# Kernel tuning notes

Measured on AMD Instinct MI355X. Metric: run time of the kernel, lower is better.

## Reference

```python
import jax, jax.numpy as jnp
import numpy as np

B, C_IN, C_OUT = 4, 8, 8
P_IN, P_OUT = 16384, 4096
N_EVAL = 1_000_000
SPATIAL = 2
HID = 64
DECAY = (P_IN / 16) ** 2  # 1048576.0; bump support: ||z||^4 <= 1/DECAY -> ||z|| <= 1/32


def setup_inputs() -> dict:
    key = jax.random.key(0)
    ks = jax.random.split(key, 8)
    features = jax.random.normal(ks[0], (B, C_IN, P_IN), jnp.float32)
    # offsets inside the bump support (max ||z|| ~ 0.0283 < 0.03125 keeps 1 - DECAY*||z||^4 > 0)
    eval_locs = (jax.random.uniform(ks[1], (N_EVAL, SPATIAL), jnp.float32) * 2.0 - 1.0) * 0.02
    quad_weights = jax.random.uniform(ks[2], (P_IN,), jnp.float32, 0.5, 1.5) / P_IN
    # filter MLP: spatial_dim -> 64 -> 64 -> C_IN*C_OUT, Sin activations, no bias
    W0 = jax.random.normal(ks[3], (SPATIAL, HID), jnp.float32) / np.float32(np.sqrt(SPATIAL))
    W1 = jax.random.normal(ks[4], (HID, HID), jnp.float32) / np.float32(np.sqrt(HID))
    W2 = jax.random.normal(ks[5], (HID, C_IN * C_OUT), jnp.float32) / np.float32(np.sqrt(HID))
    eval_idx_out = jnp.sort(jax.random.randint(ks[6], (N_EVAL,), 0, P_OUT, jnp.int32))
    eval_idx_in = jax.random.randint(ks[7], (N_EVAL,), 0, P_IN, jnp.int32)
    return dict(features=features, eval_locs=eval_locs, quad_weights=quad_weights,
                W0=W0, W1=W1, W2=W2, eval_idx_out=eval_idx_out, eval_idx_in=eval_idx_in)


def reference(features, eval_locs, quad_weights, W0, W1, W2, eval_idx_out, eval_idx_in):
    # per-eval-point filter G(z): (N, C_in, C_out)
    h = jnp.sin(eval_locs @ W0)
    h = jnp.sin(h @ W1)
    filt = (h @ W2).reshape(-1, C_IN, C_OUT)
    # bump(z) = exp(1 - 1/(1 - decay*||z||^4))
    r4 = jnp.sum(eval_locs * eval_locs, axis=-1) ** 2          # (N,)
    bump = jnp.exp(1.0 - 1.0 / (1.0 - DECAY * r4))             # (N,)
    w = bump * quad_weights[eval_idx_in]                       # (N,)
    gathered = features[:, :, eval_idx_in]                     # (B, C_in, N)
    # fused bump/quad weighting + per-point matmul
    values = jnp.einsum('n,bin,nij->nbj', w, gathered, filt)   # (N, B, C_out)
    # scatter-reduce sum over output-point index
    integral = jax.ops.segment_sum(values, eval_idx_out, num_segments=P_OUT)  # (P_out, B, C_out)
    return jnp.transpose(integral, (1, 2, 0))                  # (B, C_out, P_out)
```

## Files before the change

### kernel.cpp

```cpp
#include <hip/hip_runtime.h>

#define NEV   1000000
#define POUT  4096
#define PIN   16384

typedef __bf16 bf16x8 __attribute__((ext_vector_type(8)));
typedef float  f32x16 __attribute__((ext_vector_type(16)));

#define SEG_OFF   0
#define FT_OFF    4160
#define FT_FLOATS (32 * PIN)

#define LH_ST 36
#define LW_ST 36

#define SEL_HI 0x07060302u
#define SEL_LO 0x05040100u

__device__ __forceinline__ unsigned pack_hl(float v) {
    const unsigned b = __builtin_bit_cast(unsigned, v);
    const float hb = __builtin_bit_cast(float, b & 0xFFFF0000u);
    const float lo = v - hb;
    return __builtin_amdgcn_perm(b, __builtin_bit_cast(unsigned, lo), SEL_HI);
}

#define GEMM3(accv, ahi_, alo_, bhi_, blo_)                                          \
    accv = __builtin_amdgcn_mfma_f32_32x32x16_bf16(ahi_, bhi_, accv, 0, 0, 0);       \
    accv = __builtin_amdgcn_mfma_f32_32x32x16_bf16(ahi_, blo_, accv, 0, 0, 0);       \
    accv = __builtin_amdgcn_mfma_f32_32x32x16_bf16(alo_, bhi_, accv, 0, 0, 0);

__global__ __launch_bounds__(256) void prep_k(const float* __restrict__ f,
                                              const int* __restrict__ eio,
                                              float* __restrict__ ws) {
    const int bid = blockIdx.x, t = threadIdx.x;
    if (bid < 512) {
        __shared__ float tile[32][33];
        const int p0 = bid * 32;
        #pragma unroll
        for (int rep = 0; rep < 4; ++rep) {
            const int idx = rep * 256 + t;
            const int c = idx >> 5, pl = idx & 31;
            tile[pl][c] = f[c * PIN + p0 + pl];
        }
        __syncthreads();
        #pragma unroll
        for (int rep = 0; rep < 4; ++rep) {
            const int idx = rep * 256 + t;
            const int pl = idx >> 5, c = idx & 31;
            ws[FT_OFF + (p0 + pl) * 32 + c] = tile[pl][c];
        }
    } else {
        int* seg = (int*)ws + SEG_OFF;
        const int q = (bid - 512) * 256 + t;
        int lo = 0, hi = NEV;
        while (lo < hi) { int m = (lo + hi) >> 1; if (eio[m] < q) lo = m + 1; else hi = m; }
        seg[q] = lo;
        if (q == 0) seg[POUT] = NEV;
    }
}

template <int MODE>
__global__ __launch_bounds__(256, 2) void quadconv_mfma_k(
    const float* __restrict__ features,
    const float* __restrict__ eval_locs,
    const float* __restrict__ quad_weights,
    const float* __restrict__ W0,
    const float* __restrict__ W1,
    const float* __restrict__ W2,
    const int* __restrict__ eio,
    const int* __restrict__ eii,
    const float* __restrict__ ws,
    float* __restrict__ out)
{
    __shared__ unsigned lh[4][64 * LH_ST];
    __shared__ unsigned lw[4][32 * LW_ST];
    const int tid  = threadIdx.x;
    const int wid  = tid >> 6;
    const int lane = tid & 63;
    const int n    = lane & 31;
    const int hl   = lane >> 5;
    const int p    = blockIdx.x * 4 + wid;

    int start, end;
    if constexpr (MODE == 0) {
        const int* seg = (const int*)ws + SEG_OFF;
        start = seg[p]; end = seg[p + 1];
    } else {
        int lo = 0, hi = NEV;
        while (lo < hi) { int m = (lo + hi) >> 1; if (eio[m] < p) lo = m + 1; else hi = m; }
        start = lo; hi = NEV;
        while (lo < hi) { int m = (lo + hi) >> 1; if (eio[m] <= p) lo = m + 1; else hi = m; }
        end = lo;
    }

    bf16x8 a1hi[2][4], a1lo[2][4];
    #pragma unroll
    for (int mb = 0; mb < 2; ++mb) {
        #pragma unroll
        for (int t = 0; t < 4; ++t) {
            unsigned hw[4], lw_[4];
            #pragma unroll
            for (int i = 0; i < 4; ++i) {
                const float v0 = W1[(8 * hl + 2 * i + 16 * t) * 64 + n + 32 * mb];
                const float v1 = W1[(8 * hl + 2 * i + 1 + 16 * t) * 64 + n + 32 * mb];
                const unsigned b0 = __builtin_bit_cast(unsigned, v0);
                const unsigned b1 = __builtin_bit_cast(unsigned, v1);
                const float l0 = v0 - __builtin_bit_cast(float, b0 & 0xFFFF0000u);
                const float l1 = v1 - __builtin_bit_cast(float, b1 & 0xFFFF0000u);
                hw[i]  = __builtin_amdgcn_perm(b1, b0, SEL_HI);
                lw_[i] = __builtin_amdgcn_perm(__builtin_bit_cast(unsigned, l1),
                                               __builtin_bit_cast(unsigned, l0), SEL_HI);
            }
            a1hi[mb][t] = __builtin_bit_cast(bf16x8, make_uint4(hw[0], hw[1], hw[2], hw[3]));
            a1lo[mb][t] = __builtin_bit_cast(bf16x8, make_uint4(lw_[0], lw_[1], lw_[2], lw_[3]));
        }
    }

    f32x16 T[2];
    #pragma unroll
    for (int mb = 0; mb < 2; ++mb)
        #pragma unroll
        for (int r = 0; r < 16; ++r) T[mb][r] = 0.f;

    unsigned* Lhw = &lh[wid][4 * hl * LH_ST + n];
    unsigned* Lww = &lw[wid][16 * hl * LW_ST + n];
    const unsigned* Lhr = &lh[wid][n * LH_ST + 8 * hl];
    const unsigned* Lwr = &lw[wid][n * LW_ST + 8 * hl];

    const int nt = (end - start + 31) >> 5;

    for (int tile = 0; tile < nt; ++tile) {
        const int e  = start + tile * 32 + n;
        const bool valid = (e < end);
        const int ec = valid ? e : (end - 1);
        const float2 x = ((const float2*)eval_locs)[ec];
        const int ii = eii[ec];

        const float r2 = x.x * x.x + x.y * x.y;
        const float dd = 1.0f - 1048576.0f * r2 * r2;
        float wgt = __expf(1.0f - 1.0f / dd) * quad_weights[ii];
        if (!valid) wgt = 0.f;

        f32x16 acc1[2];
        #pragma unroll
        for (int mb = 0; mb < 2; ++mb)
            #pragma unroll
            for (int r = 0; r < 16; ++r) acc1[mb][r] = 0.f;

        #pragma unroll
        for (int t = 0; t < 4; ++t) {
            const int k0 = 16 * t + 8 * hl;
            float s[8];
            #pragma unroll
            for (int q = 0; q < 8; ++q)
                s[q] = __sinf(fmaf(x.x, W0[k0 + q], x.y * W0[64 + k0 + q]));
            unsigned hw[4], lw_[4];
            #pragma unroll
            for (int i = 0; i < 4; ++i) {
                const unsigned b0 = __builtin_bit_cast(unsigned, s[2 * i]);
                const unsigned b1 = __builtin_bit_cast(unsigned, s[2 * i + 1]);
                const float l0 = s[2 * i]     - __builtin_bit_cast(float, b0 & 0xFFFF0000u);
                const float l1 = s[2 * i + 1] - __builtin_bit_cast(float, b1 & 0xFFFF0000u);
                hw[i]  = __builtin_amdgcn_perm(b1, b0, SEL_HI);
                lw_[i] = __builtin_amdgcn_perm(__builtin_bit_cast(unsigned, l1),
                                               __builtin_bit_cast(unsigned, l0), SEL_HI);
            }
            const bf16x8 bhi = __builtin_bit_cast(bf16x8, make_uint4(hw[0], hw[1], hw[2], hw[3]));
            const bf16x8 blo = __builtin_bit_cast(bf16x8, make_uint4(lw_[0], lw_[1], lw_[2], lw_[3]));
            GEMM3(acc1[0], a1hi[0][t], a1lo[0][t], bhi, blo);
            GEMM3(acc1[1], a1hi[1][t], a1lo[1][t], bhi, blo);
        }

        #pragma unroll
        for (int mb = 0; mb < 2; ++mb) {
            #pragma unroll
            for (int r = 0; r < 16; ++r) {
                const int row = ((r & 3) + 8 * (r >> 2) + 32 * mb);
                Lhw[row * LH_ST] = pack_hl(__sinf(acc1[mb][r]));
            }
        }

        {
            float g[16];
            if constexpr (MODE == 0) {
                const float4* gp = (const float4*)(ws + FT_OFF + ii * 32 + 16 * hl);
                const float4 G0 = gp[0], G1 = gp[1], G2 = gp[2], G3 = gp[3];
                g[0]=G0.x; g[1]=G0.y; g[2]=G0.z; g[3]=G0.w;
                g[4]=G1.x; g[5]=G1.y; g[6]=G1.z; g[7]=G1.w;
                g[8]=G2.x; g[9]=G2.y; g[10]=G2.z; g[11]=G2.w;
                g[12]=G3.x; g[13]=G3.y; g[14]=G3.z; g[15]=G3.w;
            } else {
                #pragma unroll
                for (int v = 0; v < 16; ++v) g[v] = features[(16 * hl + v) * PIN + ii];
            }
            #pragma unroll
            for (int v = 0; v < 16; ++v) Lww[v * LW_ST] = pack_hl(wgt * g[v]);
        }

        #pragma unroll
        for (int kt = 0; kt < 2; ++kt) {
            const uint4 p0 = *(const uint4*)(Lwr + 16 * kt);
            const uint4 p1 = *(const uint4*)(Lwr + 16 * kt + 4);
            const bf16x8 bh = __builtin_bit_cast(bf16x8, make_uint4(
                __builtin_amdgcn_perm(p0.y, p0.x, SEL_HI),
                __builtin_amdgcn_perm(p0.w, p0.z, SEL_HI),
                __builtin_amdgcn_perm(p1.y, p1.x, SEL_HI),
                __builtin_amdgcn_perm(p1.w, p1.z, SEL_HI)));
            const bf16x8 bl = __builtin_bit_cast(bf16x8, make_uint4(
                __builtin_amdgcn_perm(p0.y, p0.x, SEL_LO),
                __builtin_amdgcn_perm(p0.w, p0.z, SEL_LO),
                __builtin_amdgcn_perm(p1.y, p1.x, SEL_LO),
                __builtin_amdgcn_perm(p1.w, p1.z, SEL_LO)));
            #pragma unroll
            for (int mb = 0; mb < 2; ++mb) {
                const uint4 q0 = *(const uint4*)(Lhr + 32 * mb * LH_ST + 16 * kt);
                const uint4 q1 = *(const uint4*)(Lhr + 32 * mb * LH_ST + 16 * kt + 4);
                const bf16x8 ah = __builtin_bit_cast(bf16x8, make_uint4(
                    __builtin_amdgcn_perm(q0.y, q0.x, SEL_HI),
                    __builtin_amdgcn_perm(q0.w, q0.z, SEL_HI),
                    __builtin_amdgcn_perm(q1.y, q1.x, SEL_HI),
                    __builtin_amdgcn_perm(q1.w, q1.z, SEL_HI)));
                const bf16x8 al = __builtin_bit_cast(bf16x8, make_uint4(
                    __builtin_amdgcn_perm(q0.y, q0.x, SEL_LO),
                    __builtin_amdgcn_perm(q0.w, q0.z, SEL_LO),
                    __builtin_amdgcn_perm(q1.y, q1.x, SEL_LO),
                    __builtin_amdgcn_perm(q1.w, q1.z, SEL_LO)));
                GEMM3(T[mb], ah, al, bh, bl);
            }
        }
    }

    {
        const int i = n & 7, b = n >> 3;
        float pj[8];
        #pragma unroll
        for (int j = 0; j < 8; ++j) pj[j] = 0.f;
        #pragma unroll
        for (int mb = 0; mb < 2; ++mb) {
            #pragma unroll
            for (int r = 0; r < 16; ++r) {
                const int khid = (r & 3) + 8 * (r >> 2) + 4 * hl + 32 * mb;
                const float tv = T[mb][r];
                const float4 w20 = *(const float4*)(W2 + khid * 64 + i * 8);
                const float4 w21 = *(const float4*)(W2 + khid * 64 + i * 8 + 4);
                pj[0] = fmaf(tv, w20.x, pj[0]);
                pj[1] = fmaf(tv, w20.y, pj[1]);
                pj[2] = fmaf(tv, w20.z, pj[2]);
                pj[3] = fmaf(tv, w20.w, pj[3]);
                pj[4] = fmaf(tv, w21.x, pj[4]);
                pj[5] = fmaf(tv, w21.y, pj[5]);
                pj[6] = fmaf(tv, w21.z, pj[6]);
                pj[7] = fmaf(tv, w21.w, pj[7]);
            }
        }
        #pragma unroll
        for (int j = 0; j < 8; ++j) {
            float v = pj[j];
            v += __shfl_xor(v, 1);
            v += __shfl_xor(v, 2);
            v += __shfl_xor(v, 4);
            v += __shfl_xor(v, 32);
            pj[j] = v;
        }
        if (i == 0 && hl == 0) {
            #pragma unroll
            for (int j = 0; j < 8; ++j) out[b * (8 * POUT) + j * POUT + p] = pj[j];
        }
    }
}

extern "C" void kernel_launch(void* const* d_in, const int* in_sizes, int n_in,
                              void* d_out, int out_size, void* d_ws, size_t ws_size,
                              hipStream_t stream) {
    const float* features  = (const float*)d_in[0];
    const float* eval_locs = (const float*)d_in[1];
    const float* qw        = (const float*)d_in[2];
    const float* W0        = (const float*)d_in[3];
    const float* W1        = (const float*)d_in[4];
    const float* W2        = (const float*)d_in[5];
    const int*   eio       = (const int*)d_in[6];
    const int*   eii       = (const int*)d_in[7];
    float* out = (float*)d_out;
    float* ws  = (float*)d_ws;

    const size_t need0 = (size_t)(FT_OFF + FT_FLOATS) * 4;
    if (ws_size >= need0) {
        prep_k<<<512 + POUT / 256, 256, 0, stream>>>(features, eio, ws);
        quadconv_mfma_k<0><<<POUT / 4, 256, 0, stream>>>(features, eval_locs, qw, W0, W1, W2,
                                                         eio, eii, ws, out);
    } else {
        quadconv_mfma_k<2><<<POUT / 4, 256, 0, stream>>>(features, eval_locs, qw, W0, W1, W2,
                                                         eio, eii, ws, out);
    }
}
```

Before: 140.2 us.

## Use one-wave blocks, in-kernel segment search, and hardware sin with pre-scaled weights

The main kernel now launches one 64-thread wave per output point instead of four waves per 256-thread block, with launch bounds (64,3). The separate segment-boundary binary search in the prep kernel is dropped; each wave instead does two parallel lane searches and broadcasts start and end with shuffles. The sines now call the hardware sin builtin, which takes its input in revolutions, with W1 and the eval coordinates pre-scaled by 1/(2π) so no extra multiply is needed per call. This aims to improve scheduling granularity and load balance and to cut sine cost, at the risk of more small blocks and a longer per-wave prologue.

```diff
diff --git a/kernel.cpp b/kernel.cpp
--- a/kernel.cpp
+++ b/kernel.cpp
@@ -1,14 +1,13 @@
 #include <hip/hip_runtime.h>
 
-#define NEV   1000000
-#define POUT  4096
-#define PIN   16384
+#define NEV    1000000
+#define POUT   4096
+#define PIN    16384
+#define INV2PI 0.15915494309189535f
 
 typedef __bf16 bf16x8 __attribute__((ext_vector_type(8)));
 typedef float  f32x16 __attribute__((ext_vector_type(16)));
 
-#define SEG_OFF   0
-#define FT_OFF    4160
 #define FT_FLOATS (32 * PIN)
 
 #define LH_ST 36
@@ -30,37 +29,27 @@
     accv = __builtin_amdgcn_mfma_f32_32x32x16_bf16(alo_, bhi_, accv, 0, 0, 0);
 
 __global__ __launch_bounds__(256) void prep_k(const float* __restrict__ f,
-                                              const int* __restrict__ eio,
                                               float* __restrict__ ws) {
-    const int bid = blockIdx.x, t = threadIdx.x;
-    if (bid < 512) {
-        __shared__ float tile[32][33];
-        const int p0 = bid * 32;
-        #pragma unroll
-        for (int rep = 0; rep < 4; ++rep) {
-            const int idx = rep * 256 + t;
-            const int c = idx >> 5, pl = idx & 31;
-            tile[pl][c] = f[c * PIN + p0 + pl];
-        }
-        __syncthreads();
-        #pragma unroll
-        for (int rep = 0; rep < 4; ++rep) {
-            const int idx = rep * 256 + t;
-            const int pl = idx >> 5, c = idx & 31;
-            ws[FT_OFF + (p0 + pl) * 32 + c] = tile[pl][c];
-        }
-    } else {
-        int* seg = (int*)ws + SEG_OFF;
-        const int q = (bid - 512) * 256 + t;
-        int lo = 0, hi = NEV;
-        while (lo < hi) { int m = (lo + hi) >> 1; if (eio[m] < q) lo = m + 1; else hi = m; }
-        seg[q] = lo;
-        if (q == 0) seg[POUT] = NEV;
+    __shared__ float tile[32][33];
+    const int t = threadIdx.x;
+    const int p0 = blockIdx.x * 32;
+    #pragma unroll
+    for (int rep = 0; rep < 4; ++rep) {
+        const int idx = rep * 256 + t;
+        const int c = idx >> 5, pl = idx & 31;
+        tile[pl][c] = f[c * PIN + p0 + pl];
+    }
+    __syncthreads();
+    #pragma unroll
+    for (int rep = 0; rep < 4; ++rep) {
+        const int idx = rep * 256 + t;
+        const int pl = idx >> 5, c = idx & 31;
+        ws[(p0 + pl) * 32 + c] = tile[pl][c];
     }
 }
 
 template <int MODE>
-__global__ __launch_bounds__(256, 2) void quadconv_mfma_k(
+__global__ __launch_bounds__(64, 3) void quadconv_mfma_k(
     const float* __restrict__ features,
     const float* __restrict__ eval_locs,
     const float* __restrict__ quad_weights,
@@ -72,25 +61,20 @@
     const float* __restrict__ ws,
     float* __restrict__ out)
 {
-    __shared__ unsigned lh[4][64 * LH_ST];
-    __shared__ unsigned lw[4][32 * LW_ST];
-    const int tid  = threadIdx.x;
-    const int wid  = tid >> 6;
-    const int lane = tid & 63;
+    __shared__ unsigned lh[64 * LH_ST];
+    __shared__ unsigned lw[32 * LW_ST];
+    const int lane = threadIdx.x;
     const int n    = lane & 31;
     const int hl   = lane >> 5;
-    const int p    = blockIdx.x * 4 + wid;
+    const int p    = blockIdx.x;
 
     int start, end;
-    if constexpr (MODE == 0) {
-        const int* seg = (const int*)ws + SEG_OFF;
-        start = seg[p]; end = seg[p + 1];
-    } else {
+    {
+        const int tgt = p + (lane & 1);
         int lo = 0, hi = NEV;
-        while (lo < hi) { int m = (lo + hi) >> 1; if (eio[m] < p) lo = m + 1; else hi = m; }
-        start = lo; hi = NEV;
-        while (lo < hi) { int m = (lo + hi) >> 1; if (eio[m] <= p) lo = m + 1; else hi = m; }
-        end = lo;
+        while (lo < hi) { int m = (lo + hi) >> 1; if (eio[m] < tgt) lo = m + 1; else hi = m; }
+        start = __shfl(lo, 0);
+        end   = __shfl(lo, 1);
     }
 
     bf16x8 a1hi[2][4], a1lo[2][4];
@@ -101,8 +85,8 @@
             unsigned hw[4], lw_[4];
             #pragma unroll
             for (int i = 0; i < 4; ++i) {
-                const float v0 = W1[(8 * hl + 2 * i + 16 * t) * 64 + n + 32 * mb];
-                const float v1 = W1[(8 * hl + 2 * i + 1 + 16 * t) * 64 + n + 32 * mb];
+                const float v0 = W1[(8 * hl + 2 * i + 16 * t) * 64 + n + 32 * mb] * INV2PI;
+                const float v1 = W1[(8 * hl + 2 * i + 1 + 16 * t) * 64 + n + 32 * mb] * INV2PI;
                 const unsigned b0 = __builtin_bit_cast(unsigned, v0);
                 const unsigned b1 = __builtin_bit_cast(unsigned, v1);
                 const float l0 = v0 - __builtin_bit_cast(float, b0 & 0xFFFF0000u);
@@ -122,10 +106,10 @@
         #pragma unroll
         for (int r = 0; r < 16; ++r) T[mb][r] = 0.f;
 
-    unsigned* Lhw = &lh[wid][4 * hl * LH_ST + n];
-    unsigned* Lww = &lw[wid][16 * hl * LW_ST + n];
-    const unsigned* Lhr = &lh[wid][n * LH_ST + 8 * hl];
-    const unsigned* Lwr = &lw[wid][n * LW_ST + 8 * hl];
+    unsigned* Lhw = &lh[4 * hl * LH_ST + n];
+    unsigned* Lww = &lw[16 * hl * LW_ST + n];
+    const unsigned* Lhr = &lh[n * LH_ST + 8 * hl];
+    const unsigned* Lwr = &lw[n * LW_ST + 8 * hl];
 
     const int nt = (end - start + 31) >> 5;
 
@@ -141,6 +125,9 @@
         float wgt = __expf(1.0f - 1.0f / dd) * quad_weights[ii];
         if (!valid) wgt = 0.f;
 
+        const float xs = x.x * INV2PI;
+        const float ys = x.y * INV2PI;
+
         f32x16 acc1[2];
         #pragma unroll
         for (int mb = 0; mb < 2; ++mb)
@@ -153,7 +140,7 @@
             float s[8];
             #pragma unroll
             for (int q = 0; q < 8; ++q)
-                s[q] = __sinf(fmaf(x.x, W0[k0 + q], x.y * W0[64 + k0 + q]));
+                s[q] = __builtin_amdgcn_sinf(fmaf(xs, W0[k0 + q], ys * W0[64 + k0 + q]));
             unsigned hw[4], lw_[4];
             #pragma unroll
             for (int i = 0; i < 4; ++i) {
@@ -176,14 +163,14 @@
             #pragma unroll
             for (int r = 0; r < 16; ++r) {
                 const int row = ((r & 3) + 8 * (r >> 2) + 32 * mb);
-                Lhw[row * LH_ST] = pack_hl(__sinf(acc1[mb][r]));
+                Lhw[row * LH_ST] = pack_hl(__builtin_amdgcn_sinf(acc1[mb][r]));
             }
         }
 
         {
             float g[16];
             if constexpr (MODE == 0) {
-                const float4* gp = (const float4*)(ws + FT_OFF + ii * 32 + 16 * hl);
+                const float4* gp = (const float4*)(ws + ii * 32 + 16 * hl);
                 const float4 G0 = gp[0], G1 = gp[1], G2 = gp[2], G3 = gp[3];
                 g[0]=G0.x; g[1]=G0.y; g[2]=G0.z; g[3]=G0.w;
                 g[4]=G1.x; g[5]=G1.y; g[6]=G1.z; g[7]=G1.w;
@@ -283,13 +270,12 @@
     float* out = (float*)d_out;
     float* ws  = (float*)d_ws;
 
-    const size_t need0 = (size_t)(FT_OFF + FT_FLOATS) * 4;
-    if (ws_size >= need0) {
-        prep_k<<<512 + POUT / 256, 256, 0, stream>>>(features, eio, ws);
-        quadconv_mfma_k<0><<<POUT / 4, 256, 0, stream>>>(features, eval_locs, qw, W0, W1, W2,
-                                                         eio, eii, ws, out);
+    if (ws_size >= (size_t)FT_FLOATS * 4) {
+        prep_k<<<PIN / 32, 256, 0, stream>>>(features, ws);
+        quadconv_mfma_k<0><<<POUT, 64, 0, stream>>>(features, eval_locs, qw, W0, W1, W2,
+                                                    eio, eii, ws, out);
     } else {
-        quadconv_mfma_k<2><<<POUT / 4, 256, 0, stream>>>(features, eval_locs, qw, W0, W1, W2,
-                                                         eio, eii, ws, out);
-    }
-}
+        quadconv_mfma_k<2><<<POUT, 64, 0, stream>>>(features, eval_locs, qw, W0, W1, W2,
+                                                    eio, eii, ws, out);
+    }
+}
```

Measured after the change: 237.0 us. 69.1% more time.
